# Performance work log

Measured on AMD Instinct MI355X. Metric: run time of the kernel, lower is better.

## Reference

```python
import jax, jax.numpy as jnp
import numpy as np

N_NODES = 50000
N_EDGES = 400000
N_FEAT = 128
HIDDEN = 128
N_HEADS = 4
HEADC = HIDDEN // N_HEADS  # 32
N_CLASSES = 10
K_HOPS = 3
CST = 1e-5


def setup_inputs() -> dict:
    key = jax.random.key(0)
    ks = jax.random.split(key, 12)
    s = 1.0 / np.sqrt(HIDDEN)
    return {
        "node_feat": jax.random.normal(ks[0], (N_NODES, N_FEAT), jnp.float32),
        "edge_index": jax.random.randint(ks[1], (2, N_EDGES), 0, N_NODES, jnp.int64),
        # Linear weights stored as [in, out] so forward is x @ W + b
        "Wt": jax.random.normal(ks[2], (N_FEAT, HIDDEN), jnp.float32) / np.sqrt(N_FEAT),
        "bt": jax.random.normal(ks[3], (HIDDEN,), jnp.float32) * 0.01,
        "Wq": jax.random.normal(ks[4], (HIDDEN, N_HEADS * HEADC), jnp.float32) * s,
        "bq": jax.random.normal(ks[5], (N_HEADS * HEADC,), jnp.float32) * 0.01,
        "Wk": jax.random.normal(ks[6], (HIDDEN, N_HEADS * HEADC), jnp.float32) * s,
        "bk": jax.random.normal(ks[7], (N_HEADS * HEADC,), jnp.float32) * 0.01,
        "Wv": jax.random.normal(ks[8], (HIDDEN, N_HEADS * N_CLASSES), jnp.float32) * s,
        "bv": jax.random.normal(ks[9], (N_HEADS * N_CLASSES,), jnp.float32) * 0.01,
        "hopwise": jnp.ones((K_HOPS + 1,), jnp.float32),          # Parameter(ones(K+1))
        "headwise": jax.random.normal(ks[10], (N_HEADS, K_HOPS), jnp.float32) * 0.1,  # Parameter, zeros at init; randomized for testing
    }


def reference(node_feat, edge_index, Wt, bt, Wq, bq, Wk, bk, Wv, bv, hopwise, headwise):
    N = node_feat.shape[0]
    row, col = edge_index[0], edge_index[1]

    # eval mode: dropout is identity
    x = jax.nn.relu(node_feat @ Wt + bt)                       # [N, hidden]
    Q = (1.0 + jax.nn.elu(x @ Wq + bq)).reshape(N, N_HEADS, HEADC)
    Kf = (1.0 + jax.nn.elu(x @ Wk + bk)).reshape(N, N_HEADS, HEADC)
    V = (x @ Wv + bv).reshape(N, N_HEADS, N_CLASSES)

    M = jnp.einsum('nhi,nhj->nhij', Kf, V)                     # [N, H, headc, C]
    hidden = V * hopwise[0]                                     # ind_gamma & gamma_softmax branch
    layerwise = jax.nn.softmax(headwise, axis=0)                # softmax over heads (dim=-2)

    for hop in range(K_HOPS):
        # PyG sum aggregation, source_to_target: out[col] += x[row]
        M = jax.ops.segment_sum(M[row], col, num_segments=N)
        Kf = jax.ops.segment_sum(Kf[row], col, num_segments=N)
        H = jnp.einsum('nhi,nhij->nhj', Q, M)                  # [N, H, C]
        C = jnp.einsum('nhi,nhi->nh', Q, Kf)[..., None] + CST  # [N, H, 1]
        H = H / C
        gamma = hopwise[hop + 1] * layerwise[:, hop][:, None]  # [H, 1]
        hidden = hidden + gamma * H

    return hidden.sum(axis=-2)                                  # multi_concat=False: sum over heads -> [N, C]
```

## Files before the change

### kernel.cpp

```cpp
#include <hip/hip_runtime.h>
#include <hip/hip_bf16.h>

#define NN 50000
#define NE 400000
#define NF 128
#define HID 128
#define NH 4
#define HC 32
#define NC 10
#define KHOPS 3
#define NBLK ((NN + 1023) / 1024)

typedef unsigned int uint;
typedef unsigned short ushort;
typedef __attribute__((ext_vector_type(8))) short bf16x8;
typedef __attribute__((ext_vector_type(4))) float f32x4;
typedef __attribute__((ext_vector_type(2))) float f32x2;

__global__ void detect_kernel(const int* __restrict__ ei, int* __restrict__ flag) {
    int w = ei[2 * threadIdx.x + 1];
    unsigned long long b = __ballot(w != 0);
    if (threadIdx.x == 0) *flag = (b == 0ULL) ? 1 : 0;
}

__device__ __forceinline__ int edge_row(const int* ei, int is64, int e) {
    return is64 ? ei[2 * e] : ei[e];
}
__device__ __forceinline__ int edge_col(const int* ei, int is64, int e) {
    return is64 ? ei[2 * NE + 2 * e] : ei[NE + e];
}

__global__ void zero_kernel(int* __restrict__ p, int n) {
    int i = blockIdx.x * blockDim.x + threadIdx.x;
    if (i < n) p[i] = 0;
}

__global__ void hist_kernel(const int* __restrict__ ei, const int* __restrict__ flag,
                            int* __restrict__ counts) {
    int e = blockIdx.x * blockDim.x + threadIdx.x;
    if (e >= NE) return;
    int c = edge_col(ei, *flag, e);
    atomicAdd(&counts[c], 1);
}

__global__ __launch_bounds__(256) void bsum_kernel(const int* __restrict__ counts,
                                                   int* __restrict__ bsum) {
    int b = blockIdx.x, tid = threadIdx.x;
    int base = b * 1024 + tid * 4;
    int4 v = {0, 0, 0, 0};
    if (base < NN) v = *(const int4*)(counts + base);
    int s = v.x + v.y + v.z + v.w;
#pragma unroll
    for (int off = 32; off >= 1; off >>= 1) s += __shfl_xor(s, off);
    __shared__ int ws[4];
    int lane = tid & 63, w = tid >> 6;
    if (lane == 0) ws[w] = s;
    __syncthreads();
    if (tid == 0) bsum[b] = ws[0] + ws[1] + ws[2] + ws[3];
}

__global__ void bscan_kernel(const int* __restrict__ bsum, int* __restrict__ boff,
                             int* __restrict__ rowptr) {
    int lane = threadIdx.x;
    int v = (lane < NBLK) ? bsum[lane] : 0;
    int t = v;
#pragma unroll
    for (int off = 1; off < 64; off <<= 1) {
        int u = __shfl_up(t, off);
        if (lane >= off) t += u;
    }
    if (lane < NBLK) boff[lane] = t - v;
    if (lane == NBLK - 1) rowptr[NN] = t;
}

__global__ __launch_bounds__(256) void scanb_kernel(const int* __restrict__ counts,
                                                    const int* __restrict__ boff,
                                                    int* __restrict__ rowptr,
                                                    int* __restrict__ cursor) {
    int b = blockIdx.x, tid = threadIdx.x;
    int base = b * 1024 + tid * 4;
    int4 v = {0, 0, 0, 0};
    if (base < NN) v = *(const int4*)(counts + base);
    int s3 = v.x + v.y + v.z + v.w;
    int lane = tid & 63, w = tid >> 6;
    int t = s3;
#pragma unroll
    for (int off = 1; off < 64; off <<= 1) {
        int u = __shfl_up(t, off);
        if (lane >= off) t += u;
    }
    __shared__ int ws[4];
    if (lane == 63) ws[w] = t;
    __syncthreads();
    int wofs = boff[b];
    for (int i = 0; i < 4; i++) wofs += (i < w) ? ws[i] : 0;
    int excl = wofs + t - s3;
    if (base < NN) {
        int4 o;
        o.x = excl;
        o.y = excl + v.x;
        o.z = o.y + v.y;
        o.w = o.z + v.z;
        *(int4*)(rowptr + base) = o;
        *(int4*)(cursor + base) = o;
    }
}

__global__ void scatter_kernel(const int* __restrict__ ei, const int* __restrict__ flag,
                               int* __restrict__ cursor, int* __restrict__ srows) {
    int e = blockIdx.x * blockDim.x + threadIdx.x;
    if (e >= NE) return;
    int is64 = *flag;
    int r = edge_row(ei, is64, e);
    int c = edge_col(ei, is64, e);
    int pos = atomicAdd(&cursor[c], 1);
    srows[pos] = r;
}

__device__ __forceinline__ short bfbits(float f) {
    __hip_bfloat16 h = __float2bfloat16(f);
    return *reinterpret_cast<short*>(&h);
}
__device__ __forceinline__ ushort bfbitsu(float f) {
    __hip_bfloat16 h = __float2bfloat16(f);
    return *reinterpret_cast<ushort*>(&h);
}
__device__ __forceinline__ float bfs(ushort u) { return __uint_as_float(((uint)u) << 16); }
__device__ __forceinline__ f32x2 bf2(uint u) {
    return f32x2{__uint_as_float(u << 16), __uint_as_float(u & 0xFFFF0000u)};
}

template<bool HI>
__device__ __forceinline__ uint pk8(float a, float b, uint old) {
    return __builtin_amdgcn_cvt_pk_fp8_f32(a, b, old, HI);
}
template<bool HI>
__device__ __forceinline__ f32x2 upk8(uint w) {
    return __builtin_amdgcn_cvt_pk_f32_fp8(w, HI);
}

__global__ void wconv_kernel(const float* __restrict__ Wt, const float* __restrict__ Wq,
                             const float* __restrict__ Wk, const float* __restrict__ Wv,
                             ushort* __restrict__ Wtb, ushort* __restrict__ Wqkvb) {
    int idx = blockIdx.x * 256 + threadIdx.x;
    if (idx < 128 * 128) {
        int c = idx >> 7, k = idx & 127;
        Wtb[c * 128 + k] = bfbitsu(Wt[k * 128 + c]);
    }
    if (idx < 304 * 128) {
        int c = idx >> 7, k = idx & 127;
        float w;
        if (c < 128) w = Wq[k * 128 + c];
        else if (c < 256) w = Wk[k * 128 + (c - 128)];
        else { int cv = c - 256; w = (cv < 40) ? Wv[k * 40 + cv] : 0.f; }
        Wqkvb[c * 128 + k] = bfbitsu(w);
    }
}

__global__ __launch_bounds__(256) void xm_kernel(const float* __restrict__ nf,
                                                 const ushort* __restrict__ Wtb,
                                                 const float* __restrict__ bt,
                                                 ushort* __restrict__ xb) {
    int wid = threadIdx.x >> 6, lane = threadIdx.x & 63;
    int row0 = blockIdx.x * 64 + wid * 16;
    int r = lane & 15, kg = lane >> 4;
    int ar = row0 + r;
    if (ar > NN - 1) ar = NN - 1;
    int ctbeg = blockIdx.y * 4;
    f32x4 acc[4];
#pragma unroll
    for (int ct = 0; ct < 4; ct++) acc[ct] = f32x4{0.f, 0.f, 0.f, 0.f};
#pragma unroll
    for (int ks = 0; ks < 4; ks++) {
        int k0 = ks * 32 + kg * 8;
        const float4* ap = (const float4*)(nf + (size_t)ar * 128 + k0);
        float4 a0 = ap[0], a1 = ap[1];
        bf16x8 af;
        af[0] = bfbits(a0.x); af[1] = bfbits(a0.y); af[2] = bfbits(a0.z); af[3] = bfbits(a0.w);
        af[4] = bfbits(a1.x); af[5] = bfbits(a1.y); af[6] = bfbits(a1.z); af[7] = bfbits(a1.w);
#pragma unroll
        for (int ct = 0; ct < 4; ct++) {
            bf16x8 bfr = *(const bf16x8*)(Wtb + (size_t)((ctbeg + ct) * 16 + r) * 128 + k0);
            acc[ct] = __builtin_amdgcn_mfma_f32_16x16x32_bf16(af, bfr, acc[ct], 0, 0, 0);
        }
    }
#pragma unroll
    for (int ct = 0; ct < 4; ct++) {
        int c = (ctbeg + ct) * 16 + r;
        float b = bt[c];
#pragma unroll
        for (int reg = 0; reg < 4; reg++) {
            int n = row0 + kg * 4 + reg;
            if (n < NN) {
                float z = acc[ct][reg] + b;
                xb[(size_t)n * 128 + c] = bfbitsu(fmaxf(z, 0.f));
            }
        }
    }
}

template<int CTBEG, int NCT>
__device__ __forceinline__ void qkv_body(const ushort* __restrict__ xb,
                                         const ushort* __restrict__ Wqkvb,
                                         const float* __restrict__ bq,
                                         const float* __restrict__ bk,
                                         const float* __restrict__ bv,
                                         float* __restrict__ Qp,
                                         unsigned char* __restrict__ K8,
                                         ushort* __restrict__ Vbf,
                                         int row0, int r, int kg) {
    int ar = row0 + r;
    if (ar > NN - 1) ar = NN - 1;
    f32x4 acc[NCT];
#pragma unroll
    for (int ct = 0; ct < NCT; ct++) acc[ct] = f32x4{0.f, 0.f, 0.f, 0.f};
#pragma unroll
    for (int ks = 0; ks < 4; ks++) {
        int k0 = ks * 32 + kg * 8;
        bf16x8 af = *(const bf16x8*)(xb + (size_t)ar * 128 + k0);
#pragma unroll
        for (int ct = 0; ct < NCT; ct++) {
            bf16x8 bfr = *(const bf16x8*)(Wqkvb + (size_t)((CTBEG + ct) * 16 + r) * 128 + k0);
            acc[ct] = __builtin_amdgcn_mfma_f32_16x16x32_bf16(af, bfr, acc[ct], 0, 0, 0);
        }
    }
#pragma unroll
    for (int ct = 0; ct < NCT; ct++) {
        int c = (CTBEG + ct) * 16 + r;
        float bias;
        if (c < 128) bias = bq[c];
        else if (c < 256) bias = bk[c - 128];
        else { int cv = c - 256; bias = (cv < 40) ? bv[cv] : 0.f; }
#pragma unroll
        for (int reg = 0; reg < 4; reg++) {
            int n = row0 + kg * 4 + reg;
            if (n >= NN) continue;
            float z = acc[ct][reg] + bias;
            if (c < 128) {
                float q = z > 0.f ? 1.f + z : __expf(z);
                Qp[(size_t)n * 128 + c] = q;
            } else if (c < 256) {
                int cc = c - 128;
                float kv = (z > 0.f ? 1.f + z : __expf(z)) * 0.0625f;
                uint w = pk8<false>(kv, 0.f, 0u);
                K8[(size_t)n * 128 + cc] = (unsigned char)(w & 0xFF);
            } else {
                int cv = c - 256;
                if (cv < 40) {
                    int hh = cv / 10, cc = cv - hh * 10;
                    Vbf[(size_t)n * 64 + hh * 16 + cc] = bfbitsu(z);
                }
            }
        }
    }
}

__global__ __launch_bounds__(256) void qkv_kernel(const ushort* __restrict__ xb,
                                                  const ushort* __restrict__ Wqkvb,
                                                  const float* __restrict__ bq,
                                                  const float* __restrict__ bk,
                                                  const float* __restrict__ bv,
                                                  float* __restrict__ Qp,
                                                  unsigned char* __restrict__ K8,
                                                  ushort* __restrict__ Vbf) {
    int wid = threadIdx.x >> 6, lane = threadIdx.x & 63;
    int row0 = blockIdx.x * 64 + wid * 16;
    int r = lane & 15, kg = lane >> 4;
    if (blockIdx.y == 0)
        qkv_body<0, 8>(xb, Wqkvb, bq, bk, bv, Qp, K8, Vbf, row0, r, kg);
    else if (blockIdx.y == 1)
        qkv_body<8, 8>(xb, Wqkvb, bq, bk, bv, Qp, K8, Vbf, row0, r, kg);
    else
        qkv_body<16, 3>(xb, Wqkvb, bq, bk, bv, Qp, K8, Vbf, row0, r, kg);
}

__device__ __forceinline__ void fused_epilog(f32x2 A0[5], f32x2 A1[5], f32x2 kA,
                                             int gw, int lane,
                                             const float* __restrict__ Qp,
                                             float* __restrict__ out,
                                             uint4* __restrict__ Mq4n, uint* __restrict__ Mrun,
                                             ushort* __restrict__ K8n,
                                             const float* __restrict__ hopwise,
                                             const float* __restrict__ headwise,
                                             const ushort* __restrict__ Vbf_all,
                                             int hop, int write_next, int is_hop0) {
    int p0 = lane * 2;
    float2 q = *(const float2*)(Qp + (size_t)gw * 128 + p0);
    float num[10];
#pragma unroll
    for (int j = 0; j < 5; j++) {
        num[2 * j] = q.x * A0[j].x + q.y * A1[j].x;
        num[2 * j + 1] = q.x * A0[j].y + q.y * A1[j].y;
    }
    float den = q.x * kA.x + q.y * kA.y;
#pragma unroll
    for (int off = 8; off >= 1; off >>= 1) {
#pragma unroll
        for (int c = 0; c < 10; c++) num[c] += __shfl_xor(num[c], off);
        den += __shfl_xor(den, off);
    }
    float e0 = __expf(headwise[0 * KHOPS + hop]);
    float e1 = __expf(headwise[1 * KHOPS + hop]);
    float e2 = __expf(headwise[2 * KHOPS + hop]);
    float e3 = __expf(headwise[3 * KHOPS + hop]);
    int h = lane >> 4;
    float eh = (h == 0) ? e0 : (h == 1) ? e1 : (h == 2) ? e2 : e3;
    float gamma = hopwise[hop + 1] * eh / (e0 + e1 + e2 + e3);
    float s = gamma / (den + 6.25e-7f);
    float tot[10];
#pragma unroll
    for (int c = 0; c < 10; c++) {
        tot[c] = s * num[c];
        tot[c] += __shfl_xor(tot[c], 16);
        tot[c] += __shfl_xor(tot[c], 32);
    }
    if (lane < 10) {
        float v = lane == 0 ? tot[0] : lane == 1 ? tot[1] : lane == 2 ? tot[2] :
                  lane == 3 ? tot[3] : lane == 4 ? tot[4] : lane == 5 ? tot[5] :
                  lane == 6 ? tot[6] : lane == 7 ? tot[7] : lane == 8 ? tot[8] : tot[9];
        if (is_hop0) {
            const ushort* vb = Vbf_all + (size_t)gw * 64 + lane;
            float vsum = bfs(vb[0]) + bfs(vb[16]) + bfs(vb[32]) + bfs(vb[48]);
            out[(size_t)gw * 10 + lane] = hopwise[0] * vsum + v;
        } else {
            out[(size_t)gw * 10 + lane] += v;
        }
    }
    if (write_next) {
        uint4 o;
        o.x = pk8<true>(A0[1].x, A0[1].y, pk8<false>(A0[0].x, A0[0].y, 0u));
        o.y = pk8<true>(A0[3].x, A0[3].y, pk8<false>(A0[2].x, A0[2].y, 0u));
        o.z = pk8<true>(A1[1].x, A1[1].y, pk8<false>(A1[0].x, A1[0].y, 0u));
        o.w = pk8<true>(A1[3].x, A1[3].y, pk8<false>(A1[2].x, A1[2].y, 0u));
        Mq4n[(size_t)gw * 64 + lane] = o;
        Mrun[(size_t)gw * 64 + lane] =
            pk8<true>(A1[4].x, A1[4].y, pk8<false>(A0[4].x, A0[4].y, 0u));
        uint kw = pk8<false>(kA.x, kA.y, 0u);
        K8n[(size_t)gw * 64 + lane] = (ushort)(kw & 0xFFFF);
    }
}

__device__ __forceinline__ void edge_acc(f32x2 A0[5], f32x2 A1[5], f32x2& kA,
                                         uint4 mq, uint mr, uint kk) {
    A0[0] += upk8<false>(mq.x);
    A0[1] += upk8<true>(mq.x);
    A0[2] += upk8<false>(mq.y);
    A0[3] += upk8<true>(mq.y);
    A1[0] += upk8<false>(mq.z);
    A1[1] += upk8<true>(mq.z);
    A1[2] += upk8<false>(mq.w);
    A1[3] += upk8<true>(mq.w);
    A0[4] += upk8<false>(mr);
    A1[4] += upk8<true>(mr);
    kA += upk8<false>(kk);
}

__global__ __launch_bounds__(256) void aggf0_kernel(const ushort* __restrict__ K8c,
                                                    const ushort* __restrict__ Vbf,
                                                    const float* __restrict__ Qp,
                                                    float* __restrict__ out,
                                                    uint4* __restrict__ Mq4n, uint* __restrict__ Mrun,
                                                    ushort* __restrict__ K8n,
                                                    const int* __restrict__ rowptr,
                                                    const int* __restrict__ srows,
                                                    const float* __restrict__ hopwise,
                                                    const float* __restrict__ headwise) {
    int gw = (blockIdx.x * 256 + threadIdx.x) >> 6;
    int lane = threadIdx.x & 63;
    int h = lane >> 4;
    int beg = rowptr[gw], end = rowptr[gw + 1];
    f32x2 A0[5], A1[5], kA = f32x2{0.f, 0.f};
#pragma unroll
    for (int j = 0; j < 5; j++) { A0[j] = f32x2{0.f, 0.f}; A1[j] = f32x2{0.f, 0.f}; }
    int e = beg;
    for (; e + 1 < end; e += 2) {
        int s0 = srows[e], s1 = srows[e + 1];
        uint k0w = K8c[(size_t)s0 * 64 + lane];
        uint k1w = K8c[(size_t)s1 * 64 + lane];
        const ushort* vb0 = Vbf + (size_t)s0 * 64 + h * 16;
        const ushort* vb1 = Vbf + (size_t)s1 * 64 + h * 16;
        uint4 v40 = *(const uint4*)vb0; uint v10 = *(const uint*)(vb0 + 8);
        uint4 v41 = *(const uint4*)vb1; uint v11 = *(const uint*)(vb1 + 8);
        f32x2 kk0 = upk8<false>(k0w);
        f32x2 kk1 = upk8<false>(k1w);
        kA += kk0 + kk1;
        f32x2 V0[5] = {bf2(v40.x), bf2(v40.y), bf2(v40.z), bf2(v40.w), bf2(v10)};
        f32x2 V1[5] = {bf2(v41.x), bf2(v41.y), bf2(v41.z), bf2(v41.w), bf2(v11)};
        f32x2 k00 = f32x2{kk0.x, kk0.x}, k01 = f32x2{kk0.y, kk0.y};
        f32x2 k10 = f32x2{kk1.x, kk1.x}, k11 = f32x2{kk1.y, kk1.y};
#pragma unroll
        for (int j = 0; j < 5; j++) {
            A0[j] += k00 * V0[j] + k10 * V1[j];
            A1[j] += k01 * V0[j] + k11 * V1[j];
        }
    }
    for (; e < end; ++e) {
        int s0 = srows[e];
        uint k0w = K8c[(size_t)s0 * 64 + lane];
        const ushort* vb0 = Vbf + (size_t)s0 * 64 + h * 16;
        uint4 v40 = *(const uint4*)vb0; uint v10 = *(const uint*)(vb0 + 8);
        f32x2 kk0 = upk8<false>(k0w);
        kA += kk0;
        f32x2 V0[5] = {bf2(v40.x), bf2(v40.y), bf2(v40.z), bf2(v40.w), bf2(v10)};
        f32x2 k00 = f32x2{kk0.x, kk0.x}, k01 = f32x2{kk0.y, kk0.y};
#pragma unroll
        for (int j = 0; j < 5; j++) {
            A0[j] += k00 * V0[j];
            A1[j] += k01 * V0[j];
        }
    }
    fused_epilog(A0, A1, kA, gw, lane, Qp, out, Mq4n, Mrun, K8n,
                 hopwise, headwise, Vbf, 0, 1, 1);
}

__global__ __launch_bounds__(256) void aggf_kernel(const uint4* __restrict__ Mq4,
                                                   const uint* __restrict__ Mru,
                                                   const ushort* __restrict__ K8c,
                                                   const float* __restrict__ Qp,
                                                   float* __restrict__ out,
                                                   uint4* __restrict__ Mq4n, uint* __restrict__ Mrun,
                                                   ushort* __restrict__ K8n,
                                                   const int* __restrict__ rowptr,
                                                   const int* __restrict__ srows,
                                                   const float* __restrict__ hopwise,
                                                   const float* __restrict__ headwise,
                                                   int hop, int write_next) {
    int gw = (blockIdx.x * 256 + threadIdx.x) >> 6;
    int lane = threadIdx.x & 63;
    int beg = rowptr[gw], end = rowptr[gw + 1];
    f32x2 A0[5], A1[5], kA = f32x2{0.f, 0.f};
#pragma unroll
    for (int j = 0; j < 5; j++) { A0[j] = f32x2{0.f, 0.f}; A1[j] = f32x2{0.f, 0.f}; }
    int e = beg;
    for (; e + 3 < end; e += 4) {
        int s0 = srows[e], s1 = srows[e + 1], s2 = srows[e + 2], s3 = srows[e + 3];
        uint4 m0 = Mq4[(size_t)s0 * 64 + lane];
        uint4 m1 = Mq4[(size_t)s1 * 64 + lane];
        uint4 m2 = Mq4[(size_t)s2 * 64 + lane];
        uint4 m3 = Mq4[(size_t)s3 * 64 + lane];
        uint r0 = Mru[(size_t)s0 * 64 + lane];
        uint r1 = Mru[(size_t)s1 * 64 + lane];
        uint r2 = Mru[(size_t)s2 * 64 + lane];
        uint r3 = Mru[(size_t)s3 * 64 + lane];
        uint k0 = K8c[(size_t)s0 * 64 + lane];
        uint k1 = K8c[(size_t)s1 * 64 + lane];
        uint k2 = K8c[(size_t)s2 * 64 + lane];
        uint k3 = K8c[(size_t)s3 * 64 + lane];
        edge_acc(A0, A1, kA, m0, r0, k0);
        edge_acc(A0, A1, kA, m1, r1, k1);
        edge_acc(A0, A1, kA, m2, r2, k2);
        edge_acc(A0, A1, kA, m3, r3, k3);
    }
    for (; e < end; ++e) {
        int s0 = srows[e];
        uint4 m0 = Mq4[(size_t)s0 * 64 + lane];
        uint r0 = Mru[(size_t)s0 * 64 + lane];
        uint k0 = K8c[(size_t)s0 * 64 + lane];
        edge_acc(A0, A1, kA, m0, r0, k0);
    }
    fused_epilog(A0, A1, kA, gw, lane, Qp, out, Mq4n, Mrun, K8n,
                 hopwise, headwise, nullptr, hop, write_next, 0);
}

extern "C" void kernel_launch(void* const* d_in, const int* in_sizes, int n_in,
                              void* d_out, int out_size, void* d_ws, size_t ws_size,
                              hipStream_t stream) {
    const float* nf = (const float*)d_in[0];
    const int* ei = (const int*)d_in[1];
    const float* Wt = (const float*)d_in[2];
    const float* bt = (const float*)d_in[3];
    const float* Wq = (const float*)d_in[4];
    const float* bq = (const float*)d_in[5];
    const float* Wk = (const float*)d_in[6];
    const float* bk = (const float*)d_in[7];
    const float* Wv = (const float*)d_in[8];
    const float* bv = (const float*)d_in[9];
    const float* hopwise = (const float*)d_in[10];
    const float* headwise = (const float*)d_in[11];
    float* out = (float*)d_out;

    char* p = (char*)d_ws;
    auto alloc = [&](size_t bytes) {
        char* r = p;
        p += (bytes + 255) & ~(size_t)255;
        return r;
    };
    int* rowptr = (int*)alloc((NN + 4) * sizeof(int));
    int* cursor = (int*)alloc((NN + 4) * sizeof(int));
    int* bsum = (int*)alloc(NBLK * sizeof(int));
    int* boff = (int*)alloc(NBLK * sizeof(int));
    int* srows = (int*)alloc((size_t)NE * sizeof(int));
    int* flag = (int*)alloc(sizeof(int));
    ushort* Wtb = (ushort*)alloc(128 * 128 * sizeof(ushort));
    ushort* Wqkvb = (ushort*)alloc(304 * 128 * sizeof(ushort));
    float* Qp = (float*)alloc((size_t)NN * 128 * sizeof(float));
    unsigned char* K8pp = (unsigned char*)alloc((size_t)NN * 128);
    ushort* Vbf = (ushort*)alloc((size_t)NN * 64 * sizeof(ushort));
    ushort* K8a = (ushort*)alloc((size_t)NN * 64 * sizeof(ushort));
    uint4* Mq4a = (uint4*)alloc((size_t)NN * 64 * sizeof(uint4));
    uint4* Mq4b = (uint4*)alloc((size_t)NN * 64 * sizeof(uint4));
    uint* Mrua = (uint*)alloc((size_t)NN * 64 * sizeof(uint));
    uint* Mrub = (uint*)alloc((size_t)NN * 64 * sizeof(uint));
    ushort* xb = (ushort*)Mq4a;
    ushort* K8b = (ushort*)K8pp;

    detect_kernel<<<1, 64, 0, stream>>>(ei, flag);
    zero_kernel<<<(NN + 255) / 256, 256, 0, stream>>>(cursor, NN);
    hist_kernel<<<(NE + 255) / 256, 256, 0, stream>>>(ei, flag, cursor);
    bsum_kernel<<<NBLK, 256, 0, stream>>>(cursor, bsum);
    bscan_kernel<<<1, 64, 0, stream>>>(bsum, boff, rowptr);
    scanb_kernel<<<NBLK, 256, 0, stream>>>(cursor, boff, rowptr, cursor);
    scatter_kernel<<<(NE + 255) / 256, 256, 0, stream>>>(ei, flag, cursor, srows);

    wconv_kernel<<<(304 * 128 + 255) / 256, 256, 0, stream>>>(Wt, Wq, Wk, Wv, Wtb, Wqkvb);
    int nrb = (NN + 63) / 64;
    xm_kernel<<<dim3(nrb, 2), 256, 0, stream>>>(nf, Wtb, bt, xb);
    qkv_kernel<<<dim3(nrb, 3), 256, 0, stream>>>(xb, Wqkvb, bq, bk, bv, Qp, K8pp, Vbf);

    aggf0_kernel<<<NN / 4, 256, 0, stream>>>((const ushort*)K8pp, Vbf, Qp, out,
                                             Mq4a, Mrua, K8a,
                                             rowptr, srows, hopwise, headwise);
    aggf_kernel<<<NN / 4, 256, 0, stream>>>(Mq4a, Mrua, K8a, Qp, out, Mq4b, Mrub, K8b,
                                            rowptr, srows, hopwise, headwise, 1, 1);
    aggf_kernel<<<NN / 4, 256, 0, stream>>>(Mq4b, Mrub, K8b, Qp, out, Mq4a, Mrua, K8a,
                                            rowptr, srows, hopwise, headwise, 2, 0);
}
```

Before: 376.6 us.

## Split each node's hop aggregation across two wavefronts with half-row layout

```diff
diff --git a/kernel.cpp b/kernel.cpp
--- a/kernel.cpp
+++ b/kernel.cpp
@@ -13,6 +13,7 @@
 
 typedef unsigned int uint;
 typedef unsigned short ushort;
+typedef unsigned char uchar;
 typedef __attribute__((ext_vector_type(8))) short bf16x8;
 typedef __attribute__((ext_vector_type(4))) float f32x4;
 typedef __attribute__((ext_vector_type(2))) float f32x2;
@@ -206,7 +207,7 @@
                                          const float* __restrict__ bk,
                                          const float* __restrict__ bv,
                                          float* __restrict__ Qp,
-                                         unsigned char* __restrict__ K8,
+                                         uchar* __restrict__ K8,
                                          ushort* __restrict__ Vbf,
                                          int row0, int r, int kg) {
     int ar = row0 + r;
@@ -243,7 +244,7 @@
                 int cc = c - 128;
                 float kv = (z > 0.f ? 1.f + z : __expf(z)) * 0.0625f;
                 uint w = pk8<false>(kv, 0.f, 0u);
-                K8[(size_t)n * 128 + cc] = (unsigned char)(w & 0xFF);
+                K8[(size_t)n * 128 + cc] = (uchar)(w & 0xFF);
             } else {
                 int cv = c - 256;
                 if (cv < 40) {
@@ -261,7 +262,7 @@
                                                   const float* __restrict__ bk,
                                                   const float* __restrict__ bv,
                                                   float* __restrict__ Qp,
-                                                  unsigned char* __restrict__ K8,
+                                                  uchar* __restrict__ K8,
                                                   ushort* __restrict__ Vbf) {
     int wid = threadIdx.x >> 6, lane = threadIdx.x & 63;
     int row0 = blockIdx.x * 64 + wid * 16;
@@ -274,93 +275,12 @@
         qkv_body<16, 3>(xb, Wqkvb, bq, bk, bv, Qp, K8, Vbf, row0, r, kg);
 }
 
-__device__ __forceinline__ void fused_epilog(f32x2 A0[5], f32x2 A1[5], f32x2 kA,
-                                             int gw, int lane,
-                                             const float* __restrict__ Qp,
-                                             float* __restrict__ out,
-                                             uint4* __restrict__ Mq4n, uint* __restrict__ Mrun,
-                                             ushort* __restrict__ K8n,
-                                             const float* __restrict__ hopwise,
-                                             const float* __restrict__ headwise,
-                                             const ushort* __restrict__ Vbf_all,
-                                             int hop, int write_next, int is_hop0) {
-    int p0 = lane * 2;
-    float2 q = *(const float2*)(Qp + (size_t)gw * 128 + p0);
-    float num[10];
-#pragma unroll
-    for (int j = 0; j < 5; j++) {
-        num[2 * j] = q.x * A0[j].x + q.y * A1[j].x;
-        num[2 * j + 1] = q.x * A0[j].y + q.y * A1[j].y;
-    }
-    float den = q.x * kA.x + q.y * kA.y;
-#pragma unroll
-    for (int off = 8; off >= 1; off >>= 1) {
-#pragma unroll
-        for (int c = 0; c < 10; c++) num[c] += __shfl_xor(num[c], off);
-        den += __shfl_xor(den, off);
-    }
-    float e0 = __expf(headwise[0 * KHOPS + hop]);
-    float e1 = __expf(headwise[1 * KHOPS + hop]);
-    float e2 = __expf(headwise[2 * KHOPS + hop]);
-    float e3 = __expf(headwise[3 * KHOPS + hop]);
-    int h = lane >> 4;
-    float eh = (h == 0) ? e0 : (h == 1) ? e1 : (h == 2) ? e2 : e3;
-    float gamma = hopwise[hop + 1] * eh / (e0 + e1 + e2 + e3);
-    float s = gamma / (den + 6.25e-7f);
-    float tot[10];
-#pragma unroll
-    for (int c = 0; c < 10; c++) {
-        tot[c] = s * num[c];
-        tot[c] += __shfl_xor(tot[c], 16);
-        tot[c] += __shfl_xor(tot[c], 32);
-    }
-    if (lane < 10) {
-        float v = lane == 0 ? tot[0] : lane == 1 ? tot[1] : lane == 2 ? tot[2] :
-                  lane == 3 ? tot[3] : lane == 4 ? tot[4] : lane == 5 ? tot[5] :
-                  lane == 6 ? tot[6] : lane == 7 ? tot[7] : lane == 8 ? tot[8] : tot[9];
-        if (is_hop0) {
-            const ushort* vb = Vbf_all + (size_t)gw * 64 + lane;
-            float vsum = bfs(vb[0]) + bfs(vb[16]) + bfs(vb[32]) + bfs(vb[48]);
-            out[(size_t)gw * 10 + lane] = hopwise[0] * vsum + v;
-        } else {
-            out[(size_t)gw * 10 + lane] += v;
-        }
-    }
-    if (write_next) {
-        uint4 o;
-        o.x = pk8<true>(A0[1].x, A0[1].y, pk8<false>(A0[0].x, A0[0].y, 0u));
-        o.y = pk8<true>(A0[3].x, A0[3].y, pk8<false>(A0[2].x, A0[2].y, 0u));
-        o.z = pk8<true>(A1[1].x, A1[1].y, pk8<false>(A1[0].x, A1[0].y, 0u));
-        o.w = pk8<true>(A1[3].x, A1[3].y, pk8<false>(A1[2].x, A1[2].y, 0u));
-        Mq4n[(size_t)gw * 64 + lane] = o;
-        Mrun[(size_t)gw * 64 + lane] =
-            pk8<true>(A1[4].x, A1[4].y, pk8<false>(A0[4].x, A0[4].y, 0u));
-        uint kw = pk8<false>(kA.x, kA.y, 0u);
-        K8n[(size_t)gw * 64 + lane] = (ushort)(kw & 0xFFFF);
-    }
-}
-
-__device__ __forceinline__ void edge_acc(f32x2 A0[5], f32x2 A1[5], f32x2& kA,
-                                         uint4 mq, uint mr, uint kk) {
-    A0[0] += upk8<false>(mq.x);
-    A0[1] += upk8<true>(mq.x);
-    A0[2] += upk8<false>(mq.y);
-    A0[3] += upk8<true>(mq.y);
-    A1[0] += upk8<false>(mq.z);
-    A1[1] += upk8<true>(mq.z);
-    A1[2] += upk8<false>(mq.w);
-    A1[3] += upk8<true>(mq.w);
-    A0[4] += upk8<false>(mr);
-    A1[4] += upk8<true>(mr);
-    kA += upk8<false>(kk);
-}
-
 __global__ __launch_bounds__(256) void aggf0_kernel(const ushort* __restrict__ K8c,
                                                     const ushort* __restrict__ Vbf,
                                                     const float* __restrict__ Qp,
                                                     float* __restrict__ out,
-                                                    uint4* __restrict__ Mq4n, uint* __restrict__ Mrun,
-                                                    ushort* __restrict__ K8n,
+                                                    uint2* __restrict__ Mq2n, ushort* __restrict__ Mr2n,
+                                                    uchar* __restrict__ K82n,
                                                     const int* __restrict__ rowptr,
                                                     const int* __restrict__ srows,
                                                     const float* __restrict__ hopwise,
@@ -409,57 +329,154 @@
             A1[j] += k01 * V0[j];
         }
     }
-    fused_epilog(A0, A1, kA, gw, lane, Qp, out, Mq4n, Mrun, K8n,
-                 hopwise, headwise, Vbf, 0, 1, 1);
-}
-
-__global__ __launch_bounds__(256) void aggf_kernel(const uint4* __restrict__ Mq4,
-                                                   const uint* __restrict__ Mru,
-                                                   const ushort* __restrict__ K8c,
+    int p0 = lane * 2;
+    float2 q = *(const float2*)(Qp + (size_t)gw * 128 + p0);
+    float num[10];
+#pragma unroll
+    for (int j = 0; j < 5; j++) {
+        num[2 * j] = q.x * A0[j].x + q.y * A1[j].x;
+        num[2 * j + 1] = q.x * A0[j].y + q.y * A1[j].y;
+    }
+    float den = q.x * kA.x + q.y * kA.y;
+#pragma unroll
+    for (int off = 8; off >= 1; off >>= 1) {
+#pragma unroll
+        for (int c = 0; c < 10; c++) num[c] += __shfl_xor(num[c], off);
+        den += __shfl_xor(den, off);
+    }
+    float e0 = __expf(headwise[0 * KHOPS + 0]);
+    float e1 = __expf(headwise[1 * KHOPS + 0]);
+    float e2 = __expf(headwise[2 * KHOPS + 0]);
+    float e3 = __expf(headwise[3 * KHOPS + 0]);
+    float eh = (h == 0) ? e0 : (h == 1) ? e1 : (h == 2) ? e2 : e3;
+    float gamma = hopwise[1] * eh / (e0 + e1 + e2 + e3);
+    float s = gamma / (den + 6.25e-7f);
+    float tot[10];
+#pragma unroll
+    for (int c = 0; c < 10; c++) {
+        tot[c] = s * num[c];
+        tot[c] += __shfl_xor(tot[c], 16);
+        tot[c] += __shfl_xor(tot[c], 32);
+    }
+    if (lane < 10) {
+        float v = lane == 0 ? tot[0] : lane == 1 ? tot[1] : lane == 2 ? tot[2] :
+                  lane == 3 ? tot[3] : lane == 4 ? tot[4] : lane == 5 ? tot[5] :
+                  lane == 6 ? tot[6] : lane == 7 ? tot[7] : lane == 8 ? tot[8] : tot[9];
+        const ushort* vb = Vbf + (size_t)gw * 64 + lane;
+        float vsum = bfs(vb[0]) + bfs(vb[16]) + bfs(vb[32]) + bfs(vb[48]);
+        out[(size_t)gw * 10 + lane] = hopwise[0] * vsum + v;
+    }
+    {
+        int R = 2 * gw + (lane >> 5);
+        int lp = ((lane >> 4) & 1) * 32 + 2 * (lane & 15);
+        uint4 o;
+        o.x = pk8<true>(A0[1].x, A0[1].y, pk8<false>(A0[0].x, A0[0].y, 0u));
+        o.y = pk8<true>(A0[3].x, A0[3].y, pk8<false>(A0[2].x, A0[2].y, 0u));
+        o.z = pk8<true>(A1[1].x, A1[1].y, pk8<false>(A1[0].x, A1[0].y, 0u));
+        o.w = pk8<true>(A1[3].x, A1[3].y, pk8<false>(A1[2].x, A1[2].y, 0u));
+        *(uint4*)(Mq2n + (size_t)R * 64 + lp) = o;
+        uint rw = pk8<true>(A1[4].x, A1[4].y, pk8<false>(A0[4].x, A0[4].y, 0u));
+        *(uint*)(Mr2n + (size_t)R * 64 + lp) = rw;
+        uint kw = pk8<false>(kA.x, kA.y, 0u);
+        *(ushort*)(K82n + (size_t)R * 64 + lp) = (ushort)(kw & 0xFFFF);
+    }
+}
+
+__device__ __forceinline__ void edge_acc2(f32x2 A[5], float& kA, uint2 m, ushort r, uchar k) {
+    A[0] += upk8<false>(m.x);
+    A[1] += upk8<true>(m.x);
+    A[2] += upk8<false>(m.y);
+    A[3] += upk8<true>(m.y);
+    A[4] += upk8<false>((uint)r);
+    kA += upk8<false>((uint)k).x;
+}
+
+__global__ __launch_bounds__(256) void aggf_kernel(const uint2* __restrict__ Mq2,
+                                                   const ushort* __restrict__ Mr2,
+                                                   const uchar* __restrict__ K82,
                                                    const float* __restrict__ Qp,
                                                    float* __restrict__ out,
-                                                   uint4* __restrict__ Mq4n, uint* __restrict__ Mrun,
-                                                   ushort* __restrict__ K8n,
+                                                   uint2* __restrict__ Mq2n, ushort* __restrict__ Mr2n,
+                                                   uchar* __restrict__ K82n,
                                                    const int* __restrict__ rowptr,
                                                    const int* __restrict__ srows,
                                                    const float* __restrict__ hopwise,
                                                    const float* __restrict__ headwise,
                                                    int hop, int write_next) {
-    int gw = (blockIdx.x * 256 + threadIdx.x) >> 6;
+    int gwv = (blockIdx.x * 256 + threadIdx.x) >> 6;
+    int gw = gwv >> 1;
+    int hp = gwv & 1;
     int lane = threadIdx.x & 63;
     int beg = rowptr[gw], end = rowptr[gw + 1];
-    f32x2 A0[5], A1[5], kA = f32x2{0.f, 0.f};
-#pragma unroll
-    for (int j = 0; j < 5; j++) { A0[j] = f32x2{0.f, 0.f}; A1[j] = f32x2{0.f, 0.f}; }
+    f32x2 A[5];
+    float kA = 0.f;
+#pragma unroll
+    for (int j = 0; j < 5; j++) A[j] = f32x2{0.f, 0.f};
     int e = beg;
     for (; e + 3 < end; e += 4) {
         int s0 = srows[e], s1 = srows[e + 1], s2 = srows[e + 2], s3 = srows[e + 3];
-        uint4 m0 = Mq4[(size_t)s0 * 64 + lane];
-        uint4 m1 = Mq4[(size_t)s1 * 64 + lane];
-        uint4 m2 = Mq4[(size_t)s2 * 64 + lane];
-        uint4 m3 = Mq4[(size_t)s3 * 64 + lane];
-        uint r0 = Mru[(size_t)s0 * 64 + lane];
-        uint r1 = Mru[(size_t)s1 * 64 + lane];
-        uint r2 = Mru[(size_t)s2 * 64 + lane];
-        uint r3 = Mru[(size_t)s3 * 64 + lane];
-        uint k0 = K8c[(size_t)s0 * 64 + lane];
-        uint k1 = K8c[(size_t)s1 * 64 + lane];
-        uint k2 = K8c[(size_t)s2 * 64 + lane];
-        uint k3 = K8c[(size_t)s3 * 64 + lane];
-        edge_acc(A0, A1, kA, m0, r0, k0);
-        edge_acc(A0, A1, kA, m1, r1, k1);
-        edge_acc(A0, A1, kA, m2, r2, k2);
-        edge_acc(A0, A1, kA, m3, r3, k3);
+        size_t b0 = (size_t)(2 * s0 + hp) * 64 + lane;
+        size_t b1 = (size_t)(2 * s1 + hp) * 64 + lane;
+        size_t b2 = (size_t)(2 * s2 + hp) * 64 + lane;
+        size_t b3 = (size_t)(2 * s3 + hp) * 64 + lane;
+        uint2 m0 = Mq2[b0], m1 = Mq2[b1], m2 = Mq2[b2], m3 = Mq2[b3];
+        ushort r0 = Mr2[b0], r1 = Mr2[b1], r2 = Mr2[b2], r3 = Mr2[b3];
+        uchar k0 = K82[b0], k1 = K82[b1], k2 = K82[b2], k3 = K82[b3];
+        edge_acc2(A, kA, m0, r0, k0);
+        edge_acc2(A, kA, m1, r1, k1);
+        edge_acc2(A, kA, m2, r2, k2);
+        edge_acc2(A, kA, m3, r3, k3);
     }
     for (; e < end; ++e) {
         int s0 = srows[e];
-        uint4 m0 = Mq4[(size_t)s0 * 64 + lane];
-        uint r0 = Mru[(size_t)s0 * 64 + lane];
-        uint k0 = K8c[(size_t)s0 * 64 + lane];
-        edge_acc(A0, A1, kA, m0, r0, k0);
-    }
-    fused_epilog(A0, A1, kA, gw, lane, Qp, out, Mq4n, Mrun, K8n,
-                 hopwise, headwise, nullptr, hop, write_next, 0);
+        size_t b0 = (size_t)(2 * s0 + hp) * 64 + lane;
+        edge_acc2(A, kA, Mq2[b0], Mr2[b0], K82[b0]);
+    }
+    float q = Qp[(size_t)gw * 128 + hp * 64 + lane];
+    float num[10];
+#pragma unroll
+    for (int j = 0; j < 5; j++) {
+        num[2 * j] = q * A[j].x;
+        num[2 * j + 1] = q * A[j].y;
+    }
+    float den = q * kA;
+#pragma unroll
+    for (int off = 16; off >= 1; off >>= 1) {
+#pragma unroll
+        for (int c = 0; c < 10; c++) num[c] += __shfl_xor(num[c], off);
+        den += __shfl_xor(den, off);
+    }
+    float e0 = __expf(headwise[0 * KHOPS + hop]);
+    float e1 = __expf(headwise[1 * KHOPS + hop]);
+    float e2 = __expf(headwise[2 * KHOPS + hop]);
+    float e3 = __expf(headwise[3 * KHOPS + hop]);
+    int h = hp * 2 + (lane >> 5);
+    float eh = (h == 0) ? e0 : (h == 1) ? e1 : (h == 2) ? e2 : e3;
+    float gamma = hopwise[hop + 1] * eh / (e0 + e1 + e2 + e3);
+    float s = gamma / (den + 6.25e-7f);
+    float tot[10];
+#pragma unroll
+    for (int c = 0; c < 10; c++) {
+        tot[c] = s * num[c];
+        tot[c] += __shfl_xor(tot[c], 32);
+    }
+    if (lane < 10) {
+        float v = lane == 0 ? tot[0] : lane == 1 ? tot[1] : lane == 2 ? tot[2] :
+                  lane == 3 ? tot[3] : lane == 4 ? tot[4] : lane == 5 ? tot[5] :
+                  lane == 6 ? tot[6] : lane == 7 ? tot[7] : lane == 8 ? tot[8] : tot[9];
+        atomicAdd(&out[(size_t)gw * 10 + lane], v);
+    }
+    if (write_next) {
+        size_t b = (size_t)(2 * gw + hp) * 64 + lane;
+        uint2 o;
+        o.x = pk8<true>(A[1].x, A[1].y, pk8<false>(A[0].x, A[0].y, 0u));
+        o.y = pk8<true>(A[3].x, A[3].y, pk8<false>(A[2].x, A[2].y, 0u));
+        Mq2n[b] = o;
+        uint rw = pk8<false>(A[4].x, A[4].y, 0u);
+        Mr2n[b] = (ushort)(rw & 0xFFFF);
+        uint kw = pk8<false>(kA, 0.f, 0u);
+        K82n[b] = (uchar)(kw & 0xFF);
+    }
 }
 
 extern "C" void kernel_launch(void* const* d_in, const int* in_sizes, int n_in,
@@ -494,15 +511,15 @@
     ushort* Wtb = (ushort*)alloc(128 * 128 * sizeof(ushort));
     ushort* Wqkvb = (ushort*)alloc(304 * 128 * sizeof(ushort));
     float* Qp = (float*)alloc((size_t)NN * 128 * sizeof(float));
-    unsigned char* K8pp = (unsigned char*)alloc((size_t)NN * 128);
+    uchar* K8pp = (uchar*)alloc((size_t)NN * 128);
     ushort* Vbf = (ushort*)alloc((size_t)NN * 64 * sizeof(ushort));
-    ushort* K8a = (ushort*)alloc((size_t)NN * 64 * sizeof(ushort));
-    uint4* Mq4a = (uint4*)alloc((size_t)NN * 64 * sizeof(uint4));
-    uint4* Mq4b = (uint4*)alloc((size_t)NN * 64 * sizeof(uint4));
-    uint* Mrua = (uint*)alloc((size_t)NN * 64 * sizeof(uint));
-    uint* Mrub = (uint*)alloc((size_t)NN * 64 * sizeof(uint));
-    ushort* xb = (ushort*)Mq4a;
-    ushort* K8b = (ushort*)K8pp;
+    uchar* K82a = (uchar*)alloc((size_t)NN * 128);
+    uint2* Mq2a = (uint2*)alloc((size_t)NN * 128 * sizeof(uint2));
+    uint2* Mq2b = (uint2*)alloc((size_t)NN * 128 * sizeof(uint2));
+    ushort* Mr2a = (ushort*)alloc((size_t)NN * 128 * sizeof(ushort));
+    ushort* Mr2b = (ushort*)alloc((size_t)NN * 128 * sizeof(ushort));
+    ushort* xb = (ushort*)Mq2a;
+    uchar* K82b = K8pp;
 
     detect_kernel<<<1, 64, 0, stream>>>(ei, flag);
     zero_kernel<<<(NN + 255) / 256, 256, 0, stream>>>(cursor, NN);
@@ -518,10 +535,12 @@
     qkv_kernel<<<dim3(nrb, 3), 256, 0, stream>>>(xb, Wqkvb, bq, bk, bv, Qp, K8pp, Vbf);
 
     aggf0_kernel<<<NN / 4, 256, 0, stream>>>((const ushort*)K8pp, Vbf, Qp, out,
-                                             Mq4a, Mrua, K8a,
+                                             Mq2a, Mr2a, K82a,
                                              rowptr, srows, hopwise, headwise);
-    aggf_kernel<<<NN / 4, 256, 0, stream>>>(Mq4a, Mrua, K8a, Qp, out, Mq4b, Mrub, K8b,
+    aggf_kernel<<<NN / 2, 256, 0, stream>>>(Mq2a, Mr2a, K82a, Qp, out,
+                                            Mq2b, Mr2b, K82b,
                                             rowptr, srows, hopwise, headwise, 1, 1);
-    aggf_kernel<<<NN / 4, 256, 0, stream>>>(Mq4b, Mrub, K8b, Qp, out, Mq4a, Mrua, K8a,
+    aggf_kernel<<<NN / 2, 256, 0, stream>>>(Mq2b, Mr2b, K82b, Qp, out,
+                                            Mq2a, Mr2a, K82a,
                                             rowptr, srows, hopwise, headwise, 2, 0);
 }
```

Measured after the change: 369.8 us. About the same (-1.8%).
